# Kernel optimization log

Measured on AMD Instinct MI355X. Metric: run time of the kernel, lower is better.

## Reference

```python
import math
import jax, jax.numpy as jnp
import numpy as np


def setup_inputs() -> dict:
    key = jax.random.key(0)
    k1, k2, k3, k4 = jax.random.split(key, 4)
    B, K, D = 131072, 64, 8
    NC = D * (D + 1) // 2  # 36
    pi = jax.random.uniform(k1, (B, K), dtype=jnp.float32)
    mu = jax.random.normal(k2, (K, D), dtype=jnp.float32)
    # 'ALREADY CONSTRAINED' Cholesky entries: keep them positive (uniform),
    # +0.1 offset keeps diagonal safely away from 0 for the log.
    L_constrained = jax.random.uniform(k3, (K, NC), dtype=jnp.float32) + 0.1
    target = jax.random.normal(k4, (B, D), dtype=jnp.float32)
    return {"pi": pi, "mu": mu, "L_constrained": L_constrained, "target": target}


def reference(pi, mu, L_constrained, target):
    B, K = pi.shape
    D = mu.shape[1]
    norm_const = -0.5 * D * math.log(2.0 * math.pi)
    ti, tj = np.tril_indices(D)
    # scatter packed cholesky into dense lower-triangular (K, D, D)
    L = jnp.zeros((K, D, D), dtype=target.dtype).at[:, ti, tj].set(L_constrained)
    diff = target[:, None, :] - mu[None, :, :]          # (B, K, D)
    # batch over components, treat B as multiple RHS: L (K,D,D) @ z = b (K,D,B)
    b = jnp.transpose(diff, (1, 2, 0))                   # (K, D, B)
    z = jax.scipy.linalg.solve_triangular(L, b, lower=True)  # (K, D, B)
    M = jnp.sum(z * z, axis=1)                           # (K, B) Mahalanobis^2
    log_dets = jnp.sum(jnp.log(jnp.diagonal(L, axis1=-2, axis2=-1)), axis=-1)  # (K,)
    log_probs = norm_const - log_dets[:, None] - 0.5 * M  # (K, B)
    weighted = log_probs.T + jnp.log(pi + 1e-10)          # (B, K)
    nll = -jnp.mean(jax.scipy.special.logsumexp(weighted, axis=1))
    return nll
```

## Files before the change

### kernel.cpp

```cpp
#include <hip/hip_runtime.h>
#include <math.h>

#define B_TOTAL 131072
#define K_COMP  64
#define D_DIM   8
#define NC      36
#define CPK     48

#define NORM_CONST (-7.3515082656373815f)

__global__ void mdn_precompute(const float* __restrict__ mu,
                               const float* __restrict__ Lc,
                               float* __restrict__ coeff) {
    int k = threadIdx.x;
    if (k >= K_COMP) return;
    const float* Lk = Lc + k * NC;

    float Lf[D_DIM][D_DIM];
    float r[D_DIM];
    float logdet = 0.0f;
    int idx = 0;
#pragma unroll
    for (int i = 0; i < D_DIM; i++) {
#pragma unroll
        for (int j = 0; j <= i; j++) {
            float v = Lk[idx++];
            if (j == i) {
                r[i] = 1.0f / v;
                logdet += logf(v);
            } else {
                Lf[i][j] = v;
            }
        }
    }

    float* out = coeff + k * CPK;
    int s = 0;
#pragma unroll
    for (int i = 1; i < D_DIM; i++) {
#pragma unroll
        for (int j = 0; j < i; j++) {
            out[s++] = r[i] * Lf[i][j];
        }
    }
#pragma unroll
    for (int i = 0; i < D_DIM; i++) out[28 + i] = r[i];
#pragma unroll
    for (int i = 0; i < D_DIM; i++) out[36 + i] = mu[k * D_DIM + i];
    out[44] = NORM_CONST - logdet;
}

__global__ __launch_bounds__(256) void mdn_main(const float* __restrict__ pi,
                                                const float* __restrict__ coeff,
                                                const float* __restrict__ target,
                                                float* __restrict__ out) {
    const int b = blockIdx.x * 256 + threadIdx.x;

    const float4* tp = (const float4*)(target + (size_t)b * D_DIM);
    float4 t0 = tp[0];
    float4 t1 = tp[1];
    float t[D_DIM] = {t0.x, t0.y, t0.z, t0.w, t1.x, t1.y, t1.z, t1.w};

    const float* pib = pi + (size_t)b * K_COMP;

    float m = -INFINITY;
    float s = 0.0f;

    for (int k4 = 0; k4 < K_COMP / 4; k4++) {
        float4 p4 = *(const float4*)(pib + 4 * k4);
        float pv[4] = {p4.x, p4.y, p4.z, p4.w};
#pragma unroll
        for (int kk = 0; kk < 4; kk++) {
            const int k = 4 * k4 + kk;
            const float* c = coeff + k * CPK;

            float d[D_DIM];
#pragma unroll
            for (int i = 0; i < D_DIM; i++) d[i] = t[i] - c[36 + i];

            float z[D_DIM];
            z[0] = d[0] * c[28];
#pragma unroll
            for (int i = 1; i < D_DIM; i++) {
                float acc = d[i] * c[28 + i];
                const int sbase = i * (i - 1) / 2;
#pragma unroll
                for (int j = 0; j < i; j++) {
                    acc = fmaf(-c[sbase + j], z[j], acc);
                }
                z[i] = acc;
            }

            float M = 0.0f;
#pragma unroll
            for (int i = 0; i < D_DIM; i++) M = fmaf(z[i], z[i], M);

            float w = fmaf(-0.5f, M, c[44]) + __logf(pv[kk] + 1e-10f);

            float nm = fmaxf(m, w);
            s = s * __expf(m - nm) + __expf(w - nm);
            m = nm;
        }
    }

    float lse = m + __logf(s);

#pragma unroll
    for (int off = 32; off > 0; off >>= 1) lse += __shfl_down(lse, off);

    __shared__ float wsum[4];
    const int lane = threadIdx.x & 63;
    const int wid = threadIdx.x >> 6;
    if (lane == 0) wsum[wid] = lse;
    __syncthreads();
    if (threadIdx.x == 0) {
        float bs = wsum[0] + wsum[1] + wsum[2] + wsum[3];
        atomicAdd(out, bs * (-1.0f / (float)B_TOTAL));
    }
}

extern "C" void kernel_launch(void* const* d_in, const int* in_sizes, int n_in,
                              void* d_out, int out_size, void* d_ws, size_t ws_size,
                              hipStream_t stream) {
    const float* pi  = (const float*)d_in[0];
    const float* mu  = (const float*)d_in[1];
    const float* Lc  = (const float*)d_in[2];
    const float* tgt = (const float*)d_in[3];
    float* out   = (float*)d_out;
    float* coeff = (float*)d_ws;

    hipMemsetAsync(d_out, 0, sizeof(float), stream);
    mdn_precompute<<<1, 64, 0, stream>>>(mu, Lc, coeff);
    mdn_main<<<B_TOTAL / 256, 256, 0, stream>>>(pi, coeff, tgt, out);
}
```

Baseline: 114.4 us.

## Split mixture components across four threads per sample with two-pass logsumexp

Each sample is now handled by four threads, each covering 16 components, and the per-thread partial logsumexp results are merged with xor shuffles. The online max/rescale loop is replaced by a two-pass scheme that computes all 16 weights, takes their max, then sums pi times exp, which removes per-component logs and one exp each. This raises parallelism and the grid size fourfold, and pi reads become contiguous across the four threads. The cost is redundant target loads and more register pressure for the 16 stored weights.

```diff
diff --git a/kernel.cpp b/kernel.cpp
--- a/kernel.cpp
+++ b/kernel.cpp
@@ -6,6 +6,7 @@
 #define D_DIM   8
 #define NC      36
 #define CPK     48
+#define KPT     16
 
 #define NORM_CONST (-7.3515082656373815f)
 
@@ -50,68 +51,84 @@
     out[44] = NORM_CONST - logdet;
 }
 
-__global__ __launch_bounds__(256) void mdn_main(const float* __restrict__ pi,
-                                                const float* __restrict__ coeff,
-                                                const float* __restrict__ target,
-                                                float* __restrict__ out) {
-    const int b = blockIdx.x * 256 + threadIdx.x;
+__global__ __launch_bounds__(256, 4) void mdn_main(const float* __restrict__ pi,
+                                                   const float* __restrict__ coeff,
+                                                   const float* __restrict__ target,
+                                                   float* __restrict__ out) {
+    const int gtid = blockIdx.x * 256 + threadIdx.x;
+    const int b = gtid >> 2;
+    const int t = gtid & 3;
 
     const float4* tp = (const float4*)(target + (size_t)b * D_DIM);
     float4 t0 = tp[0];
     float4 t1 = tp[1];
-    float t[D_DIM] = {t0.x, t0.y, t0.z, t0.w, t1.x, t1.y, t1.z, t1.w};
+    float tv[D_DIM] = {t0.x, t0.y, t0.z, t0.w, t1.x, t1.y, t1.z, t1.w};
 
-    const float* pib = pi + (size_t)b * K_COMP;
+    const float* cb = coeff + (size_t)(t * KPT) * CPK;
 
+    float cw[KPT];
     float m = -INFINITY;
+
+#pragma unroll
+    for (int j = 0; j < KPT; j++) {
+        const float* c = cb + j * CPK;
+
+        float d[D_DIM];
+#pragma unroll
+        for (int i = 0; i < D_DIM; i++) d[i] = tv[i] - c[36 + i];
+
+        float z[D_DIM];
+        z[0] = d[0] * c[28];
+#pragma unroll
+        for (int i = 1; i < D_DIM; i++) {
+            float acc = d[i] * c[28 + i];
+            const int sbase = i * (i - 1) / 2;
+#pragma unroll
+            for (int jj = 0; jj < i; jj++) {
+                acc = fmaf(-c[sbase + jj], z[jj], acc);
+            }
+            z[i] = acc;
+        }
+
+        float M = 0.0f;
+#pragma unroll
+        for (int i = 0; i < D_DIM; i++) M = fmaf(z[i], z[i], M);
+
+        cw[j] = fmaf(-0.5f, M, c[44]);
+        m = fmaxf(m, cw[j]);
+    }
+
+    const float* pib = pi + (size_t)b * K_COMP + t * KPT;
     float s = 0.0f;
-
-    for (int k4 = 0; k4 < K_COMP / 4; k4++) {
-        float4 p4 = *(const float4*)(pib + 4 * k4);
+#pragma unroll
+    for (int q = 0; q < KPT / 4; q++) {
+        float4 p4 = *(const float4*)(pib + 4 * q);
         float pv[4] = {p4.x, p4.y, p4.z, p4.w};
 #pragma unroll
-        for (int kk = 0; kk < 4; kk++) {
-            const int k = 4 * k4 + kk;
-            const float* c = coeff + k * CPK;
-
-            float d[D_DIM];
-#pragma unroll
-            for (int i = 0; i < D_DIM; i++) d[i] = t[i] - c[36 + i];
-
-            float z[D_DIM];
-            z[0] = d[0] * c[28];
-#pragma unroll
-            for (int i = 1; i < D_DIM; i++) {
-                float acc = d[i] * c[28 + i];
-                const int sbase = i * (i - 1) / 2;
-#pragma unroll
-                for (int j = 0; j < i; j++) {
-                    acc = fmaf(-c[sbase + j], z[j], acc);
-                }
-                z[i] = acc;
-            }
-
-            float M = 0.0f;
-#pragma unroll
-            for (int i = 0; i < D_DIM; i++) M = fmaf(z[i], z[i], M);
-
-            float w = fmaf(-0.5f, M, c[44]) + __logf(pv[kk] + 1e-10f);
-
-            float nm = fmaxf(m, w);
-            s = s * __expf(m - nm) + __expf(w - nm);
-            m = nm;
+        for (int u = 0; u < 4; u++) {
+            s += (pv[u] + 1e-10f) * __expf(cw[4 * q + u] - m);
         }
     }
 
+#pragma unroll
+    for (int off = 1; off <= 2; off <<= 1) {
+        float mo = __shfl_xor(m, off);
+        float so = __shfl_xor(s, off);
+        float nm = fmaxf(m, mo);
+        s = s * __expf(m - nm) + so * __expf(mo - nm);
+        m = nm;
+    }
+
     float lse = m + __logf(s);
+    float val = (t == 0) ? lse : 0.0f;
 
 #pragma unroll
-    for (int off = 32; off > 0; off >>= 1) lse += __shfl_down(lse, off);
+    for (int off = 32; off > 0; off >>= 1) val += __shfl_down(val, off);
 
     __shared__ float wsum[4];
     const int lane = threadIdx.x & 63;
     const int wid = threadIdx.x >> 6;
-    if (lane == 0) wsum[wid] = lse;
+    if (lane == 0) wsum[wid] = val;
     __syncthreads();
     if (threadIdx.x == 0) {
         float bs = wsum[0] + wsum[1] + wsum[2] + wsum[3];
@@ -131,5 +148,5 @@
 
     hipMemsetAsync(d_out, 0, sizeof(float), stream);
     mdn_precompute<<<1, 64, 0, stream>>>(mu, Lc, coeff);
-    mdn_main<<<B_TOTAL / 256, 256, 0, stream>>>(pi, coeff, tgt, out);
+    mdn_main<<<(B_TOTAL * 4) / 256, 256, 0, stream>>>(pi, coeff, tgt, out);
 }
```

Result: slower. 238.2 us (+108.2%).

## Recast Mahalanobis log-probs as quadratic-feature GEMM on bf16 MFMA with split precision

Applied to the files above, without the earlier changes.

Expands each component's log density into a quadratic form in the target. Precompute builds -0.5·P, h and a constant per component, where P = L^-T L^-1, and stores them as hi/lo bf16 pairs. The main kernel forms per-row features (t_i·t_j, t, 1) and evaluates all 64 components with three-pass split-bf16 MFMA 16x16x32, then does the logsumexp with lane shuffles, multiplying by pi instead of adding log pi. This replaces per-thread scalar triangular solves with matrix-core work and removes the output memset launch. The cost is precision: the quadratic expansion can cancel badly and the split bf16 is only about 16 mantissa bits.

```diff
diff --git a/kernel.cpp b/kernel.cpp
--- a/kernel.cpp
+++ b/kernel.cpp
@@ -5,117 +5,214 @@
 #define K_COMP  64
 #define D_DIM   8
 #define NC      36
-#define CPK     48
+#define NFEAT   96
+#define ROWS_PB 128
+#define RT_PW   2
 
 #define NORM_CONST (-7.3515082656373815f)
+
+typedef __attribute__((ext_vector_type(8))) short bf16x8;
+typedef __attribute__((ext_vector_type(4))) float f32x4;
+
+static __device__ __forceinline__ unsigned short bf16_rne(float x) {
+    unsigned u = __float_as_uint(x);
+    u += 0x7FFF + ((u >> 16) & 1);
+    return (unsigned short)(u >> 16);
+}
+static __device__ __forceinline__ float bf16_f32(unsigned short h) {
+    return __uint_as_float(((unsigned)h) << 16);
+}
 
 __global__ void mdn_precompute(const float* __restrict__ mu,
                                const float* __restrict__ Lc,
-                               float* __restrict__ coeff) {
+                               unsigned short* __restrict__ psi_hi,
+                               unsigned short* __restrict__ psi_lo,
+                               float* __restrict__ out) {
     int k = threadIdx.x;
+    if (k == 0) out[0] = 0.0f;
     if (k >= K_COMP) return;
     const float* Lk = Lc + k * NC;
 
-    float Lf[D_DIM][D_DIM];
-    float r[D_DIM];
+    float L[D_DIM][D_DIM];
+    float W[D_DIM][D_DIM];
+#pragma unroll
+    for (int i = 0; i < D_DIM; i++)
+#pragma unroll
+        for (int j = 0; j < D_DIM; j++) { L[i][j] = 0.0f; W[i][j] = 0.0f; }
+
     float logdet = 0.0f;
     int idx = 0;
 #pragma unroll
-    for (int i = 0; i < D_DIM; i++) {
+    for (int i = 0; i < D_DIM; i++)
 #pragma unroll
         for (int j = 0; j <= i; j++) {
             float v = Lk[idx++];
-            if (j == i) {
-                r[i] = 1.0f / v;
-                logdet += logf(v);
-            } else {
-                Lf[i][j] = v;
+            L[i][j] = v;
+            if (j == i) logdet += logf(v);
+        }
+
+#pragma unroll
+    for (int j = 0; j < D_DIM; j++) {
+        W[j][j] = 1.0f / L[j][j];
+#pragma unroll
+        for (int i = 0; i < D_DIM; i++) {
+            if (i > j) {
+                float acc = 0.0f;
+#pragma unroll
+                for (int m = 0; m < D_DIM; m++)
+                    if (m >= j && m < i) acc += L[i][m] * W[m][j];
+                W[i][j] = -acc / L[i][i];
             }
         }
     }
 
-    float* out = coeff + k * CPK;
-    int s = 0;
-#pragma unroll
-    for (int i = 1; i < D_DIM; i++) {
-#pragma unroll
-        for (int j = 0; j < i; j++) {
-            out[s++] = r[i] * Lf[i][j];
-        }
-    }
-#pragma unroll
-    for (int i = 0; i < D_DIM; i++) out[28 + i] = r[i];
-#pragma unroll
-    for (int i = 0; i < D_DIM; i++) out[36 + i] = mu[k * D_DIM + i];
-    out[44] = NORM_CONST - logdet;
-}
-
-__global__ __launch_bounds__(256) void mdn_main(const float* __restrict__ pi,
-                                                const float* __restrict__ coeff,
-                                                const float* __restrict__ target,
-                                                float* __restrict__ out) {
-    const int b = blockIdx.x * 256 + threadIdx.x;
-
-    const float4* tp = (const float4*)(target + (size_t)b * D_DIM);
-    float4 t0 = tp[0];
-    float4 t1 = tp[1];
-    float t[D_DIM] = {t0.x, t0.y, t0.z, t0.w, t1.x, t1.y, t1.z, t1.w};
-
-    const float* pib = pi + (size_t)b * K_COMP;
-
-    float m = -INFINITY;
-    float s = 0.0f;
-
-    for (int k4 = 0; k4 < K_COMP / 4; k4++) {
-        float4 p4 = *(const float4*)(pib + 4 * k4);
-        float pv[4] = {p4.x, p4.y, p4.z, p4.w};
-#pragma unroll
-        for (int kk = 0; kk < 4; kk++) {
-            const int k = 4 * k4 + kk;
-            const float* c = coeff + k * CPK;
-
-            float d[D_DIM];
-#pragma unroll
-            for (int i = 0; i < D_DIM; i++) d[i] = t[i] - c[36 + i];
-
-            float z[D_DIM];
-            z[0] = d[0] * c[28];
-#pragma unroll
-            for (int i = 1; i < D_DIM; i++) {
-                float acc = d[i] * c[28 + i];
-                const int sbase = i * (i - 1) / 2;
-#pragma unroll
-                for (int j = 0; j < i; j++) {
-                    acc = fmaf(-c[sbase + j], z[j], acc);
-                }
-                z[i] = acc;
+    float P[D_DIM][D_DIM];
+#pragma unroll
+    for (int a = 0; a < D_DIM; a++)
+#pragma unroll
+        for (int b = 0; b < D_DIM; b++) {
+            float acc = 0.0f;
+#pragma unroll
+            for (int m = 0; m < D_DIM; m++) acc += W[m][a] * W[m][b];
+            P[a][b] = acc;
+        }
+
+    float h[D_DIM];
+    float qf = 0.0f;
+#pragma unroll
+    for (int i = 0; i < D_DIM; i++) {
+        float acc = 0.0f;
+#pragma unroll
+        for (int j = 0; j < D_DIM; j++) acc += P[i][j] * mu[k * D_DIM + j];
+        h[i] = acc;
+        qf += mu[k * D_DIM + i] * acc;
+    }
+    float g = NORM_CONST - logdet - 0.5f * qf;
+
+    float psi[NFEAT];
+#pragma unroll
+    for (int e = 0; e < NFEAT; e++) psi[e] = 0.0f;
+#pragma unroll
+    for (int a = 0; a < D_DIM; a++)
+#pragma unroll
+        for (int b = 0; b < D_DIM; b++) psi[8 * a + b] = -0.5f * P[a][b];
+#pragma unroll
+    for (int b = 0; b < D_DIM; b++) psi[64 + b] = h[b];
+    psi[72] = g;
+
+    unsigned short* oh = psi_hi + k * NFEAT;
+    unsigned short* ol = psi_lo + k * NFEAT;
+#pragma unroll
+    for (int e = 0; e < NFEAT; e++) {
+        unsigned short hi = bf16_rne(psi[e]);
+        oh[e] = hi;
+        ol[e] = bf16_rne(psi[e] - bf16_f32(hi));
+    }
+}
+
+__global__ __launch_bounds__(256, 4) void mdn_main(
+        const float* __restrict__ pi,
+        const unsigned short* __restrict__ psi_hi,
+        const unsigned short* __restrict__ psi_lo,
+        const float* __restrict__ target,
+        float* __restrict__ out) {
+    const int tid = threadIdx.x;
+    const int lane = tid & 63;
+    const int w = tid >> 6;
+    const int q = lane >> 4;
+    const int n = lane & 15;
+    const int rowbase = blockIdx.x * ROWS_PB;
+
+    __shared__ float Tl[ROWS_PB * D_DIM];
+    {
+        const float4* src = (const float4*)(target + (size_t)rowbase * D_DIM);
+        ((float4*)Tl)[tid] = src[tid];
+    }
+    __syncthreads();
+
+    float lacc = 0.0f;
+
+#pragma unroll
+    for (int r = 0; r < RT_PW; r++) {
+        const int row0 = (w * RT_PW + r) * 16;
+
+        const float4* trow = (const float4*)(Tl + (row0 + n) * D_DIM);
+        float4 tlo = trow[0], thi = trow[1];
+        float tv[D_DIM] = {tlo.x, tlo.y, tlo.z, tlo.w, thi.x, thi.y, thi.z, thi.w};
+
+        float pv[4][4];
+#pragma unroll
+        for (int reg = 0; reg < 4; reg++) {
+            const float* pr = pi + (size_t)(rowbase + row0 + 4 * q + reg) * K_COMP + n;
+#pragma unroll
+            for (int nt = 0; nt < 4; nt++) pv[reg][nt] = pr[16 * nt];
+        }
+
+        float ta0 = (q & 2) ? ((q & 1) ? tlo.w : tlo.z) : ((q & 1) ? tlo.y : tlo.x);
+        float ta1 = (q & 2) ? ((q & 1) ? thi.w : thi.z) : ((q & 1) ? thi.y : thi.x);
+
+        bf16x8 Ahi[3], Alo[3];
+#pragma unroll
+        for (int j = 0; j < D_DIM; j++) {
+            float f0 = ta0 * tv[j];
+            unsigned short h0 = bf16_rne(f0);
+            Ahi[0][j] = (short)h0;
+            Alo[0][j] = (short)bf16_rne(f0 - bf16_f32(h0));
+
+            float f1 = ta1 * tv[j];
+            unsigned short h1 = bf16_rne(f1);
+            Ahi[1][j] = (short)h1;
+            Alo[1][j] = (short)bf16_rne(f1 - bf16_f32(h1));
+
+            float f2 = (q == 0) ? tv[j] : ((q == 1 && j == 0) ? 1.0f : 0.0f);
+            unsigned short h2 = bf16_rne(f2);
+            Ahi[2][j] = (short)h2;
+            Alo[2][j] = (short)bf16_rne(f2 - bf16_f32(h2));
+        }
+
+        f32x4 acc[4];
+#pragma unroll
+        for (int nt = 0; nt < 4; nt++) {
+            const unsigned short* bh = psi_hi + ((16 * nt + n) * NFEAT + 8 * q);
+            const unsigned short* bl = psi_lo + ((16 * nt + n) * NFEAT + 8 * q);
+            f32x4 a = {0.0f, 0.0f, 0.0f, 0.0f};
+#pragma unroll
+            for (int ks = 0; ks < 3; ks++) {
+                bf16x8 Bh = *(const bf16x8*)(bh + 32 * ks);
+                bf16x8 Bl = *(const bf16x8*)(bl + 32 * ks);
+                a = __builtin_amdgcn_mfma_f32_16x16x32_bf16(Ahi[ks], Bh, a, 0, 0, 0);
+                a = __builtin_amdgcn_mfma_f32_16x16x32_bf16(Alo[ks], Bh, a, 0, 0, 0);
+                a = __builtin_amdgcn_mfma_f32_16x16x32_bf16(Ahi[ks], Bl, a, 0, 0, 0);
             }
-
-            float M = 0.0f;
-#pragma unroll
-            for (int i = 0; i < D_DIM; i++) M = fmaf(z[i], z[i], M);
-
-            float w = fmaf(-0.5f, M, c[44]) + __logf(pv[kk] + 1e-10f);
-
-            float nm = fmaxf(m, w);
-            s = s * __expf(m - nm) + __expf(w - nm);
-            m = nm;
-        }
-    }
-
-    float lse = m + __logf(s);
-
-#pragma unroll
-    for (int off = 32; off > 0; off >>= 1) lse += __shfl_down(lse, off);
-
+            acc[nt] = a;
+        }
+
+#pragma unroll
+        for (int reg = 0; reg < 4; reg++) {
+            float c0 = acc[0][reg], c1 = acc[1][reg], c2 = acc[2][reg], c3 = acc[3][reg];
+            float mrow = fmaxf(fmaxf(c0, c1), fmaxf(c2, c3));
+#pragma unroll
+            for (int off = 1; off < 16; off <<= 1)
+                mrow = fmaxf(mrow, __shfl_xor(mrow, off));
+            float s = (pv[reg][0] + 1e-10f) * __expf(c0 - mrow)
+                    + (pv[reg][1] + 1e-10f) * __expf(c1 - mrow)
+                    + (pv[reg][2] + 1e-10f) * __expf(c2 - mrow)
+                    + (pv[reg][3] + 1e-10f) * __expf(c3 - mrow);
+#pragma unroll
+            for (int off = 1; off < 16; off <<= 1)
+                s += __shfl_xor(s, off);
+            float lse = mrow + __logf(s);
+            lacc += (n == 0) ? lse : 0.0f;
+        }
+    }
+
+#pragma unroll
+    for (int off = 32; off > 0; off >>= 1) lacc += __shfl_down(lacc, off);
     __shared__ float wsum[4];
-    const int lane = threadIdx.x & 63;
-    const int wid = threadIdx.x >> 6;
-    if (lane == 0) wsum[wid] = lse;
+    if (lane == 0) wsum[w] = lacc;
     __syncthreads();
-    if (threadIdx.x == 0) {
-        float bs = wsum[0] + wsum[1] + wsum[2] + wsum[3];
-        atomicAdd(out, bs * (-1.0f / (float)B_TOTAL));
+    if (tid == 0) {
+        atomicAdd(out, (wsum[0] + wsum[1] + wsum[2] + wsum[3]) * (-1.0f / (float)B_TOTAL));
     }
 }
 
@@ -126,10 +223,11 @@
     const float* mu  = (const float*)d_in[1];
     const float* Lc  = (const float*)d_in[2];
     const float* tgt = (const float*)d_in[3];
-    float* out   = (float*)d_out;
-    float* coeff = (float*)d_ws;
-
-    hipMemsetAsync(d_out, 0, sizeof(float), stream);
-    mdn_precompute<<<1, 64, 0, stream>>>(mu, Lc, coeff);
-    mdn_main<<<B_TOTAL / 256, 256, 0, stream>>>(pi, coeff, tgt, out);
-}
+    float* out = (float*)d_out;
+
+    unsigned short* psi_hi = (unsigned short*)d_ws;
+    unsigned short* psi_lo = (unsigned short*)((char*)d_ws + K_COMP * NFEAT * 2);
+
+    mdn_precompute<<<1, 64, 0, stream>>>(mu, Lc, psi_hi, psi_lo, out);
+    mdn_main<<<B_TOTAL / ROWS_PB, 256, 0, stream>>>(pi, psi_hi, psi_lo, tgt, out);
+}
```

New measurement: 100.1 us. 12.5% less time.
